# Performance work log

Hardware: AMD Instinct MI355X
Metric: run time of the kernel (lower is better)

Reference implementation:

```python
import jax, jax.numpy as jnp
import numpy as np

H = 8          # num_heads
DM = 128       # dmodel
BN_EPS = 1e-5


def _linear(x, w, b):
    # w stored as [in, out]
    return x @ w + b


def _relu_mha(q, k, v, qw, qb, kw, kb, vw, vb, ow, ob, mask):
    """TemMulHeadAtte: ReLU on projected Q/K/V, masked softmax, ReLU out-proj.
    q,k: [B,N,T,2*DM]; v: [B,N,T,DM]; mask: broadcastable to [B,N,H,T,T] or None."""
    B, N, T, _ = q.shape
    Q = jax.nn.relu(_linear(q, qw, qb)).reshape(B, N, T, H, -1)  # e = 2*DM/H
    K = jax.nn.relu(_linear(k, kw, kb)).reshape(B, N, T, H, -1)
    V = jax.nn.relu(_linear(v, vw, vb)).reshape(B, N, T, H, -1)  # d = DM/H
    scale = 1.0 / np.sqrt(Q.shape[-1]).astype(np.float32)
    scores = jnp.einsum('bnthe,bnshe->bnhts', Q, K)
    if mask is not None:
        scores = jnp.where(mask, -jnp.inf, scores)
    attn = jax.nn.softmax(scale * scores, axis=-1)  # dropout p=0 -> identity
    out = jnp.einsum('bnhts,bnshd->bnthd', attn, V).reshape(B, N, T, -1)
    return jax.nn.relu(_linear(out, ow, ob))


def setup_inputs() -> dict:
    key = jax.random.key(0)
    ks = iter(jax.random.split(key, 32))
    B, N, T = 16, 207, 24
    def w(shape, scale=0.05):
        return (jax.random.normal(next(ks), shape, dtype=jnp.float32) * scale)
    inp = {
        'x': w((B, N, T, DM), 1.0),
        'hidden': w((B, N, T, DM), 1.0),
        'tXin': w((B, N, T, DM), 1.0),
    }
    dk = 2 * DM // H * H   # 256
    dv = DM // H * H       # 128
    for pre in ('s', 't'):  # space / temporal attention params
        inp[pre + 'q_w'] = w((2 * DM, dk)); inp[pre + 'q_b'] = w((dk,))
        inp[pre + 'k_w'] = w((2 * DM, dk)); inp[pre + 'k_b'] = w((dk,))
        inp[pre + 'v_w'] = w((DM, dv));     inp[pre + 'v_b'] = w((dv,))
        inp[pre + 'o_w'] = w((dv, DM));     inp[pre + 'o_b'] = w((DM,))
    inp['gate_w'] = w((2 * DM, DM)); inp['gate_b'] = w((DM,))
    inp['bn_gamma'] = jnp.ones((DM,), jnp.float32)
    inp['bn_beta'] = jnp.zeros((DM,), jnp.float32)
    return inp


def reference(x, hidden, tXin,
              sq_w, sq_b, sk_w, sk_b, sv_w, sv_b, so_w, so_b,
              tq_w, tq_b, tk_w, tk_b, tv_w, tv_b, to_w, to_b,
              gate_w, gate_b, bn_gamma, bn_beta):
    B, N, T, E = hidden.shape
    ht = jnp.concatenate([hidden, tXin], axis=3)  # [B,N,T,2*DM]
    # spatial attention: attend over nodes (N<->T permute)
    sqk = ht.transpose(0, 2, 1, 3)        # [B,T,N,2*DM]
    sval = hidden.transpose(0, 2, 1, 3)   # [B,T,N,DM]
    spaceOut = _relu_mha(sqk, sqk, sval, sq_w, sq_b, sk_w, sk_b, sv_w, sv_b,
                         so_w, so_b, None).transpose(0, 2, 1, 3)  # [B,N,T,DM]
    # temporal attention with causal (strict upper-tri) mask
    mask = jnp.triu(jnp.ones((T, T), dtype=bool), 1)[None, None, None]
    tempOut = _relu_mha(ht, ht, hidden, tq_w, tq_b, tk_w, tk_b, tv_w, tv_b,
                        to_w, to_b, mask)  # [B,N,T,DM]
    # gate + BatchNorm2d over channel dim (training-mode batch stats, biased var)
    gi = _linear(jnp.concatenate([spaceOut, tempOut], axis=3), gate_w, gate_b)
    mean = gi.mean(axis=(0, 1, 2))
    var = gi.var(axis=(0, 1, 2))
    z = jax.nn.sigmoid((gi - mean) * jax.lax.rsqrt(var + BN_EPS) * bn_gamma + bn_beta)
    return z * spaceOut + (1.0 - z) * tempOut
```

## Files before the change

kernel.cpp:

```cpp
#include <hip/hip_runtime.h>
#include <hip/hip_bf16.h>

typedef __bf16 bf16;
typedef __bf16 bf16x8 __attribute__((ext_vector_type(8)));
typedef float f32x4 __attribute__((ext_vector_type(4)));

#define MTOT 79488
#define NDIM 207
#define TDIM 24

__global__ void detect_dtype(const void* __restrict__ hidden, int* __restrict__ flag)
{
    __shared__ int cnt;
    if (threadIdx.x == 0) cnt = 0;
    __syncthreads();
    const bf16* h = (const bf16*)hidden;
    int local = 0;
    for (int i = threadIdx.x; i < 4096; i += 256) {
        float v = (float)h[i];
        if (!(fabsf(v) < 1e6f)) local++;
    }
    atomicAdd(&cnt, local);
    __syncthreads();
    if (threadIdx.x == 0) *flag = (cnt > 8) ? 1 : 0;
}

__device__ inline float ld_ext(const void* p, int idx, int isF32)
{
    return isF32 ? ((const float*)p)[idx] : (float)((const bf16*)p)[idx];
}

__global__ __launch_bounds__(256) void cvt_inputs(
    const void* __restrict__ hidden, const void* __restrict__ tXin,
    bf16* __restrict__ hb, bf16* __restrict__ tb, const int* __restrict__ dtf)
{
    const int isF32 = *dtf;
    const void* src = blockIdx.y ? tXin : hidden;
    bf16* dst = blockIdx.y ? tb : hb;
    const size_t e8 = ((size_t)blockIdx.x * 256 + threadIdx.x) * 8;
    bf16x8 v;
    if (isF32) {
        f32x4 lo = *(const f32x4*)((const float*)src + e8);
        f32x4 hi = *(const f32x4*)((const float*)src + e8 + 4);
        v[0]=(bf16)lo[0]; v[1]=(bf16)lo[1]; v[2]=(bf16)lo[2]; v[3]=(bf16)lo[3];
        v[4]=(bf16)hi[0]; v[5]=(bf16)hi[1]; v[6]=(bf16)hi[2]; v[7]=(bf16)hi[3];
    } else {
        v = *(const bf16x8*)((const bf16*)src + e8);
    }
    *(bf16x8*)(dst + e8) = v;
}

__global__ __launch_bounds__(256) void prep_weights(
    const void* __restrict__ sq, const void* __restrict__ sk, const void* __restrict__ sv,
    const void* __restrict__ so, const void* __restrict__ tq, const void* __restrict__ tk,
    const void* __restrict__ tv, const void* __restrict__ to_, const void* __restrict__ gw,
    const void* __restrict__ sqb, const void* __restrict__ skb, const void* __restrict__ svb,
    const void* __restrict__ sob, const void* __restrict__ tqb, const void* __restrict__ tkb,
    const void* __restrict__ tvb, const void* __restrict__ tob, const void* __restrict__ gb,
    bf16* __restrict__ wdst, bf16* __restrict__ bdst, const int* __restrict__ dtf)
{
    const int isF32 = *dtf;
    if (blockIdx.x == 1536) {
        for (int j = threadIdx.x; j < 1664; j += 256) {
            const void* src; int i2;
            if      (j < 256)  { src = sqb; i2 = j; }
            else if (j < 512)  { src = skb; i2 = j - 256; }
            else if (j < 640)  { src = svb; i2 = j - 512; }
            else if (j < 896)  { src = tqb; i2 = j - 640; }
            else if (j < 1152) { src = tkb; i2 = j - 896; }
            else if (j < 1280) { src = tvb; i2 = j - 1152; }
            else if (j < 1408) { src = sob; i2 = j - 1280; }
            else if (j < 1536) { src = tob; i2 = j - 1408; }
            else               { src = gb;  i2 = j - 1536; }
            bdst[j] = (bf16)ld_ext(src, i2, isF32);
        }
        return;
    }
    const int e = blockIdx.x * 256 + threadIdx.x;
    float v;
    if (e < 327680) {
        int br = (e >= 163840);
        int e2 = e - br * 163840;
        int n = e2 >> 8, k = e2 & 255;
        const void* qw = br ? tq : sq;
        const void* kw = br ? tk : sk;
        const void* vw = br ? tv : sv;
        if      (n < 256) v = ld_ext(qw, k * 256 + n, isF32);
        else if (n < 512) v = ld_ext(kw, k * 256 + (n - 256), isF32);
        else              v = (k < 128) ? ld_ext(vw, k * 128 + (n - 512), isF32) : 0.f;
    } else if (e < 360448) {
        int br = (e >= 344064);
        int e2 = e - 327680 - br * 16384;
        int n = e2 >> 7, k = e2 & 127;
        v = ld_ext(br ? to_ : so, k * 128 + n, isF32);
    } else {
        int e2 = e - 360448;
        int n = e2 >> 8, k = e2 & 255;
        v = ld_ext(gw, k * 128 + n, isF32);
    }
    wdst[e] = (bf16)v;
}

__global__ __launch_bounds__(256) void gemm_bt(
    const void* __restrict__ A0v, const void* __restrict__ A1v,
    const bf16* __restrict__ Bt, const bf16* __restrict__ bias,
    bf16* __restrict__ C, int Nout, int Ktot, int doRelu, int aExt,
    const int* __restrict__ dtf)
{
    const int aF32 = aExt & *dtf;
    __shared__ bf16 As[128 * 72];
    __shared__ bf16 Bs[128 * 72];
    const int tid  = threadIdx.x;
    const int wid  = tid >> 6, lane = tid & 63;
    const int wm   = (wid >> 1) * 64, wn = (wid & 1) * 64;
    const int quad = lane >> 4, l16 = lane & 15;
    const int m0   = blockIdx.x * 128, n0 = blockIdx.y * 128;
    const int lrow = tid >> 3;
    const int lcol = (tid & 7) * 8;

    f32x4 acc[4][4] = {};

    for (int k0 = 0; k0 < Ktot; k0 += 64) {
        const void* Ap = (k0 < 128) ? A0v : A1v;
        const int koff = (k0 < 128) ? k0 : k0 - 128;
        #pragma unroll
        for (int p = 0; p < 4; ++p) {
            int r = lrow + p * 32;
            bf16x8 av;
            if (aF32) {
                const float* Af = (const float*)Ap;
                f32x4 lo = *(const f32x4*)(Af + (size_t)(m0 + r) * 128 + koff + lcol);
                f32x4 hi = *(const f32x4*)(Af + (size_t)(m0 + r) * 128 + koff + lcol + 4);
                av[0]=(bf16)lo[0]; av[1]=(bf16)lo[1]; av[2]=(bf16)lo[2]; av[3]=(bf16)lo[3];
                av[4]=(bf16)hi[0]; av[5]=(bf16)hi[1]; av[6]=(bf16)hi[2]; av[7]=(bf16)hi[3];
            } else {
                av = *(const bf16x8*)((const bf16*)Ap + (size_t)(m0 + r) * 128 + koff + lcol);
            }
            *(bf16x8*)&As[r * 72 + lcol] = av;
        }
        #pragma unroll
        for (int p = 0; p < 4; ++p) {
            int r = lrow + p * 32;
            *(bf16x8*)&Bs[r * 72 + lcol] =
                *(const bf16x8*)(Bt + (size_t)(n0 + r) * Ktot + k0 + lcol);
        }
        __syncthreads();
        #pragma unroll
        for (int kk = 0; kk < 64; kk += 32) {
            bf16x8 af[4], bfr[4];
            #pragma unroll
            for (int i = 0; i < 4; ++i)
                af[i] = *(const bf16x8*)&As[(wm + i * 16 + l16) * 72 + kk + quad * 8];
            #pragma unroll
            for (int j = 0; j < 4; ++j)
                bfr[j] = *(const bf16x8*)&Bs[(wn + j * 16 + l16) * 72 + kk + quad * 8];
            #pragma unroll
            for (int i = 0; i < 4; ++i)
                #pragma unroll
                for (int j = 0; j < 4; ++j)
                    acc[i][j] = __builtin_amdgcn_mfma_f32_16x16x32_bf16(
                        af[i], bfr[j], acc[i][j], 0, 0, 0);
        }
        __syncthreads();
    }
    #pragma unroll
    for (int j = 0; j < 4; ++j) {
        int col = n0 + wn + j * 16 + l16;
        float bv = (float)bias[col];
        #pragma unroll
        for (int i = 0; i < 4; ++i) {
            int rbase = m0 + wm + i * 16 + quad * 4;
            #pragma unroll
            for (int r = 0; r < 4; ++r) {
                float v = acc[i][j][r] + bv;
                if (doRelu) v = fmaxf(v, 0.f);
                C[(size_t)(rbase + r) * Nout + col] = (bf16)v;
            }
        }
    }
}

__global__ __launch_bounds__(256) void attn_spatial_mfma(
    const bf16* __restrict__ QKV, bf16* __restrict__ O)
{
    const int hh = blockIdx.x, t = blockIdx.y, b = blockIdx.z;
    __shared__ bf16 Ks[224 * 40];
    __shared__ bf16 Vt[16 * 232];
    __shared__ bf16 Pl[4][16 * 40];
    const int tid = threadIdx.x;
    const int wave = tid >> 6, lane = tid & 63;
    const int quad = lane >> 4, l16 = lane & 15;
    const int STR = 640;

    for (int idx = tid; idx < 224 * 4; idx += 256) {
        int n = idx >> 2, seg = (idx & 3) * 8;
        bf16x8 v8 = {};
        if (n < NDIM)
            v8 = *(const bf16x8*)(QKV + ((size_t)(b * NDIM + n) * TDIM + t) * STR
                                  + 256 + hh * 32 + seg);
        *(bf16x8*)&Ks[n * 40 + seg] = v8;
    }
    for (int idx = tid; idx < 224 * 16; idx += 256) {
        int s = idx >> 4, d = idx & 15;
        bf16 v = (bf16)0.f;
        if (s < NDIM)
            v = QKV[((size_t)(b * NDIM + s) * TDIM + t) * STR + 512 + hh * 16 + d];
        Vt[d * 232 + s] = v;
    }
    __syncthreads();

    const float scale = 0.17677669529663687f;

    for (int qt = wave; qt < 13; qt += 4) {
        const int q0 = qt * 16;
        int qrow = q0 + l16; if (qrow >= NDIM) qrow = NDIM - 1;
        bf16x8 qfrag = *(const bf16x8*)(QKV + ((size_t)(b * NDIM + qrow) * TDIM + t) * STR
                                        + hh * 32 + quad * 8);
        f32x4 s[14];
        #pragma unroll
        for (int c = 0; c < 14; ++c) {
            bf16x8 kf = *(const bf16x8*)&Ks[(c * 16 + l16) * 40 + quad * 8];
            f32x4 z = {};
            s[c] = __builtin_amdgcn_mfma_f32_16x16x32_bf16(qfrag, kf, z, 0, 0, 0);
        }
        float l[4];
        #pragma unroll
        for (int r = 0; r < 4; ++r) {
            float mx = -1e30f;
            #pragma unroll
            for (int c = 0; c < 14; ++c) {
                int si = c * 16 + l16;
                float x = (si < NDIM) ? s[c][r] : -1e30f;
                mx = fmaxf(mx, x);
            }
            mx = fmaxf(mx, __shfl_xor(mx, 1));
            mx = fmaxf(mx, __shfl_xor(mx, 2));
            mx = fmaxf(mx, __shfl_xor(mx, 4));
            mx = fmaxf(mx, __shfl_xor(mx, 8));
            float sum = 0.f;
            #pragma unroll
            for (int c = 0; c < 14; ++c) {
                int si = c * 16 + l16;
                float p = (si < NDIM) ? __expf((s[c][r] - mx) * scale) : 0.f;
                s[c][r] = p;
                sum += p;
            }
            sum += __shfl_xor(sum, 1);
            sum += __shfl_xor(sum, 2);
            sum += __shfl_xor(sum, 4);
            sum += __shfl_xor(sum, 8);
            l[r] = sum;
        }
        f32x4 oacc = {};
        #pragma unroll
        for (int sc = 0; sc < 7; ++sc) {
            #pragma unroll
            for (int r = 0; r < 4; ++r) {
                Pl[wave][(quad * 4 + r) * 40 + l16]      = (bf16)s[2 * sc][r];
                Pl[wave][(quad * 4 + r) * 40 + 16 + l16] = (bf16)s[2 * sc + 1][r];
            }
            bf16x8 pf = *(const bf16x8*)&Pl[wave][l16 * 40 + quad * 8];
            bf16x8 vf = *(const bf16x8*)&Vt[l16 * 232 + sc * 32 + quad * 8];
            oacc = __builtin_amdgcn_mfma_f32_16x16x32_bf16(pf, vf, oacc, 0, 0, 0);
        }
        #pragma unroll
        for (int r = 0; r < 4; ++r) {
            int row = q0 + quad * 4 + r;
            if (row < NDIM)
                O[((size_t)(b * NDIM + row) * TDIM + t) * 128 + hh * 16 + l16]
                    = (bf16)(oacc[r] / l[r]);
        }
    }
}

__global__ __launch_bounds__(256) void attn_temporal_mfma(
    const bf16* __restrict__ QKV, bf16* __restrict__ O)
{
    const size_t m0 = (size_t)blockIdx.x * TDIM;
    __shared__ bf16 Khs[8 * 32 * 40];
    __shared__ bf16 Vts[8 * 16 * 40];
    __shared__ bf16 Pl[4][16 * 40];
    const int tid = threadIdx.x;
    const int wave = tid >> 6, lane = tid & 63;
    const int quad = lane >> 4, l16 = lane & 15;
    const int STR = 640;

    for (int idx = tid; idx < 32 * 32; idx += 256) {
        int row = idx >> 5, seg = idx & 31;
        int h = seg >> 2, j = (seg & 3) * 8;
        bf16x8 v8 = {};
        if (row < TDIM)
            v8 = *(const bf16x8*)(QKV + (m0 + row) * STR + 256 + h * 32 + j);
        *(bf16x8*)&Khs[h * 1280 + row * 40 + j] = v8;
    }
    for (int idx = tid; idx < 32 * 128; idx += 256) {
        int s = idx >> 7, c = idx & 127;
        int h = c >> 4, d = c & 15;
        bf16 v = (bf16)0.f;
        if (s < TDIM) v = QKV[(m0 + s) * STR + 512 + h * 16 + d];
        Vts[h * 640 + d * 40 + s] = v;
    }
    __syncthreads();

    const float scale = 0.17677669529663687f;

    #pragma unroll
    for (int hi = 0; hi < 2; ++hi) {
        const int h = wave * 2 + hi;
        #pragma unroll
        for (int qt = 0; qt < 2; ++qt) {
            int qrow = qt * 16 + l16; if (qrow >= TDIM) qrow = TDIM - 1;
            bf16x8 qfrag = *(const bf16x8*)(QKV + (m0 + qrow) * STR + h * 32 + quad * 8);
            bf16x8 kf0 = *(const bf16x8*)&Khs[h * 1280 + l16 * 40 + quad * 8];
            bf16x8 kf1 = *(const bf16x8*)&Khs[h * 1280 + (16 + l16) * 40 + quad * 8];
            f32x4 z = {};
            f32x4 s0 = __builtin_amdgcn_mfma_f32_16x16x32_bf16(qfrag, kf0, z, 0, 0, 0);
            f32x4 s1 = __builtin_amdgcn_mfma_f32_16x16x32_bf16(qfrag, kf1, z, 0, 0, 0);
            float l[4];
            #pragma unroll
            for (int r = 0; r < 4; ++r) {
                int q = qt * 16 + quad * 4 + r;
                float x0 = (l16 <= q) ? s0[r] : -1e30f;
                float x1 = (16 + l16 <= q && 16 + l16 < TDIM) ? s1[r] : -1e30f;
                float mx = fmaxf(x0, x1);
                mx = fmaxf(mx, __shfl_xor(mx, 1));
                mx = fmaxf(mx, __shfl_xor(mx, 2));
                mx = fmaxf(mx, __shfl_xor(mx, 4));
                mx = fmaxf(mx, __shfl_xor(mx, 8));
                float p0 = (x0 > -1e29f) ? __expf((x0 - mx) * scale) : 0.f;
                float p1 = (x1 > -1e29f) ? __expf((x1 - mx) * scale) : 0.f;
                float sum = p0 + p1;
                sum += __shfl_xor(sum, 1);
                sum += __shfl_xor(sum, 2);
                sum += __shfl_xor(sum, 4);
                sum += __shfl_xor(sum, 8);
                l[r] = sum;
                Pl[wave][(quad * 4 + r) * 40 + l16]      = (bf16)p0;
                Pl[wave][(quad * 4 + r) * 40 + 16 + l16] = (bf16)p1;
            }
            bf16x8 pf = *(const bf16x8*)&Pl[wave][l16 * 40 + quad * 8];
            bf16x8 vf = *(const bf16x8*)&Vts[h * 640 + l16 * 40 + quad * 8];
            f32x4 oacc = __builtin_amdgcn_mfma_f32_16x16x32_bf16(pf, vf, z, 0, 0, 0);
            #pragma unroll
            for (int r = 0; r < 4; ++r) {
                int row = qt * 16 + quad * 4 + r;
                if (row < TDIM)
                    O[(m0 + row) * 128 + h * 16 + l16] = (bf16)(oacc[r] / l[r]);
            }
        }
    }
}

__global__ __launch_bounds__(256) void bn_stats(
    const bf16* __restrict__ gi, float* __restrict__ stats)
{
    __shared__ float ssum[256], ssq[256];
    const size_t base = (size_t)blockIdx.x * 16384;
    const int tid = threadIdx.x;
    float s = 0.f, sq = 0.f;
    #pragma unroll 4
    for (int i = 0; i < 64; ++i) {
        float v = (float)gi[base + (size_t)i * 256 + tid];
        s += v; sq += v * v;
    }
    ssum[tid] = s; ssq[tid] = sq;
    __syncthreads();
    if (tid < 128) {
        atomicAdd(&stats[tid], ssum[tid] + ssum[tid + 128]);
        atomicAdd(&stats[128 + tid], ssq[tid] + ssq[tid + 128]);
    }
}

__global__ __launch_bounds__(256) void bn_final(
    const bf16* __restrict__ gi, const bf16* __restrict__ sp, const bf16* __restrict__ tp,
    const void* __restrict__ gammav, const void* __restrict__ betav,
    const float* __restrict__ stats, void* __restrict__ outv,
    const int* __restrict__ dtf)
{
    const int isF32 = *dtf;
    const int idx = blockIdx.x * 256 + threadIdx.x;
    const int c = idx & 127;
    const float invM = 1.f / (float)MTOT;
    float mean = stats[c] * invM;
    float var  = stats[128 + c] * invM - mean * mean;
    float gam = ld_ext(gammav, c, isF32);
    float bet = ld_ext(betav, c, isF32);
    float g = (float)gi[idx];
    float zn = (g - mean) * rsqrtf(var + 1e-5f) * gam + bet;
    float z = 1.f / (1.f + __expf(-zn));
    float s = (float)sp[idx], t = (float)tp[idx];
    float r = z * s + (1.f - z) * t;
    if (isF32) ((float*)outv)[idx] = r;
    else       ((bf16*)outv)[idx] = (bf16)r;
}

extern "C" void kernel_launch(void* const* d_in, const int* in_sizes, int n_in,
                              void* d_out, int out_size, void* d_ws, size_t ws_size,
                              hipStream_t stream)
{
    const void* hidden = d_in[1];
    const void* tXin   = d_in[2];
    const void* sq_w = d_in[3];  const void* sq_b = d_in[4];
    const void* sk_w = d_in[5];  const void* sk_b = d_in[6];
    const void* sv_w = d_in[7];  const void* sv_b = d_in[8];
    const void* so_w = d_in[9];  const void* so_b = d_in[10];
    const void* tq_w = d_in[11]; const void* tq_b = d_in[12];
    const void* tk_w = d_in[13]; const void* tk_b = d_in[14];
    const void* tv_w = d_in[15]; const void* tv_b = d_in[16];
    const void* to_w = d_in[17]; const void* to_b = d_in[18];
    const void* gate_w = d_in[19]; const void* gate_b = d_in[20];
    const void* gamma  = d_in[21]; const void* beta   = d_in[22];

    char* ws = (char*)d_ws;
    float* stats = (float*)ws;
    int*  dtf    = (int*)(ws + 1024);
    bf16* bB     = (bf16*)(ws + 2048);
    bf16* wT     = (bf16*)(ws + 8192);
    bf16* spaceO = (bf16*)(ws + 794624);
    bf16* attnO  = (bf16*)(ws + 21143552);
    bf16* QKV    = (bf16*)(ws + 41492480);
    bf16* hb     = (bf16*)(ws + 143237120);
    bf16* tb     = (bf16*)(ws + 163586048);
    bf16* tempO  = attnO;
    bf16* gi     = QKV;

    const int wsBig = (ws_size >= 184000000ull);

    bf16* sW  = wT;            bf16* tW  = wT + 163840;
    bf16* soT = wT + 327680;   bf16* toT = wT + 344064;
    bf16* gwT = wT + 360448;

    hipMemsetAsync(stats, 0, 1024, stream);
    detect_dtype<<<1, 256, 0, stream>>>(hidden, dtf);
    prep_weights<<<dim3(1537), 256, 0, stream>>>(
        sq_w, sk_w, sv_w, so_w, tq_w, tk_w, tv_w, to_w, gate_w,
        sq_b, sk_b, sv_b, so_b, tq_b, tk_b, tv_b, to_b, gate_b,
        wT, bB, dtf);
    if (wsBig)
        cvt_inputs<<<dim3(4968, 2), 256, 0, stream>>>(hidden, tXin, hb, tb, dtf);

    const void* A0 = wsBig ? (const void*)hb : hidden;
    const void* A1 = wsBig ? (const void*)tb : tXin;
    const int aExt = wsBig ? 0 : 1;

    gemm_bt<<<dim3(621, 5), 256, 0, stream>>>(A0, A1, sW, bB, QKV, 640, 256, 1, aExt, dtf);
    attn_spatial_mfma<<<dim3(8, TDIM, 16), 256, 0, stream>>>(QKV, attnO);
    gemm_bt<<<dim3(621, 1), 256, 0, stream>>>(attnO, nullptr, soT, bB + 1280, spaceO, 128, 128, 1, 0, dtf);

    gemm_bt<<<dim3(621, 5), 256, 0, stream>>>(A0, A1, tW, bB + 640, QKV, 640, 256, 1, aExt, dtf);
    attn_temporal_mfma<<<dim3(16 * NDIM), 256, 0, stream>>>(QKV, attnO);
    gemm_bt<<<dim3(621, 1), 256, 0, stream>>>(attnO, nullptr, toT, bB + 1408, tempO, 128, 128, 1, 0, dtf);

    gemm_bt<<<dim3(621, 1), 256, 0, stream>>>(spaceO, tempO, gwT, bB + 1536, gi, 128, 256, 0, 0, dtf);
    bn_stats<<<dim3(621), 256, 0, stream>>>(gi, stats);
    bn_final<<<dim3(39744), 256, 0, stream>>>(gi, spaceO, tempO, gamma, beta, stats, d_out, dtf);
}
```

Before: 545.5 us.

## Permute GEMM outputs for spatial attention, fuse BN stats, drop softmax max

The spatial QKV GEMM now writes rows in [B,T,N] order so spatial attention reads contiguous node rows and loads V with vector loads, and the out-projection GEMM scatters back to [B,N,T]. BatchNorm sum and sum-of-squares are accumulated in the gate GEMM epilogue, which removes the separate bn_stats pass. Softmax skips the max subtraction and uses exp2 and reciprocal intrinsics, padding is trimmed, and bn_final is vectorised to 8 elements per thread. Dropping the max relies on ReLU-bounded scores staying small enough not to overflow exp, and permuted scattered stores may coalesce less well.

```diff
diff --git a/kernel.cpp b/kernel.cpp
--- a/kernel.cpp
+++ b/kernel.cpp
@@ -8,6 +8,8 @@
 #define MTOT 79488
 #define NDIM 207
 #define TDIM 24
+
+#define EXP2F(x) __builtin_amdgcn_exp2f(x)
 
 __global__ void detect_dtype(const void* __restrict__ hidden, int* __restrict__ flag)
 {
@@ -105,11 +107,12 @@
     const void* __restrict__ A0v, const void* __restrict__ A1v,
     const bf16* __restrict__ Bt, const bf16* __restrict__ bias,
     bf16* __restrict__ C, int Nout, int Ktot, int doRelu, int aExt,
-    const int* __restrict__ dtf)
+    const int* __restrict__ dtf, int permMode, float* __restrict__ stats)
 {
     const int aF32 = aExt & *dtf;
     __shared__ bf16 As[128 * 72];
     __shared__ bf16 Bs[128 * 72];
+    __shared__ float lsum[128], lsq[128];
     const int tid  = threadIdx.x;
     const int wid  = tid >> 6, lane = tid & 63;
     const int wm   = (wid >> 1) * 64, wn = (wid & 1) * 64;
@@ -163,19 +166,57 @@
         }
         __syncthreads();
     }
+
+    int orow[4][4];
+    #pragma unroll
+    for (int i = 0; i < 4; ++i)
+        #pragma unroll
+        for (int r = 0; r < 4; ++r) {
+            int m = m0 + wm + i * 16 + quad * 4 + r;
+            int o;
+            if (permMode == 1) {
+                int t = m % 24, bn = m / 24;
+                int n = bn % 207, b = bn / 207;
+                o = (b * 24 + t) * 207 + n;
+            } else if (permMode == 2) {
+                int n = m % 207, bt = m / 207;
+                int t = bt % 24, b = bt / 24;
+                o = (b * 207 + n) * 24 + t;
+            } else {
+                o = m;
+            }
+            orow[i][r] = o;
+        }
+
+    if (stats) {
+        if (tid < 128) { lsum[tid] = 0.f; lsq[tid] = 0.f; }
+        __syncthreads();
+    }
     #pragma unroll
     for (int j = 0; j < 4; ++j) {
         int col = n0 + wn + j * 16 + l16;
         float bv = (float)bias[col];
+        float ps = 0.f, psq = 0.f;
         #pragma unroll
         for (int i = 0; i < 4; ++i) {
-            int rbase = m0 + wm + i * 16 + quad * 4;
             #pragma unroll
             for (int r = 0; r < 4; ++r) {
                 float v = acc[i][j][r] + bv;
                 if (doRelu) v = fmaxf(v, 0.f);
-                C[(size_t)(rbase + r) * Nout + col] = (bf16)v;
-            }
+                if (stats) { ps += v; psq += v * v; }
+                C[(size_t)orow[i][r] * Nout + col] = (bf16)v;
+            }
+        }
+        if (stats) {
+            atomicAdd(&lsum[col & 127], ps);
+            atomicAdd(&lsq[col & 127], psq);
+        }
+    }
+    if (stats) {
+        __syncthreads();
+        if (tid < 128) {
+            atomicAdd(&stats[tid], lsum[tid]);
+            atomicAdd(&stats[128 + tid], lsq[tid]);
         }
     }
 }
@@ -184,64 +225,53 @@
     const bf16* __restrict__ QKV, bf16* __restrict__ O)
 {
     const int hh = blockIdx.x, t = blockIdx.y, b = blockIdx.z;
-    __shared__ bf16 Ks[224 * 40];
+    __shared__ bf16 Ks[208 * 40];
     __shared__ bf16 Vt[16 * 232];
-    __shared__ bf16 Pl[4][16 * 40];
+    __shared__ bf16 Pl[4][2][16 * 40];
     const int tid = threadIdx.x;
     const int wave = tid >> 6, lane = tid & 63;
     const int quad = lane >> 4, l16 = lane & 15;
-    const int STR = 640;
-
-    for (int idx = tid; idx < 224 * 4; idx += 256) {
+    const size_t R = (size_t)(b * TDIM + t) * NDIM;
+
+    for (int idx = tid; idx < 832; idx += 256) {
         int n = idx >> 2, seg = (idx & 3) * 8;
         bf16x8 v8 = {};
         if (n < NDIM)
-            v8 = *(const bf16x8*)(QKV + ((size_t)(b * NDIM + n) * TDIM + t) * STR
-                                  + 256 + hh * 32 + seg);
+            v8 = *(const bf16x8*)(QKV + (R + n) * 640 + 256 + hh * 32 + seg);
         *(bf16x8*)&Ks[n * 40 + seg] = v8;
     }
-    for (int idx = tid; idx < 224 * 16; idx += 256) {
-        int s = idx >> 4, d = idx & 15;
-        bf16 v = (bf16)0.f;
+    for (int idx = tid; idx < 448; idx += 256) {
+        int s = idx >> 1, half = (idx & 1) * 8;
+        bf16x8 v8 = {};
         if (s < NDIM)
-            v = QKV[((size_t)(b * NDIM + s) * TDIM + t) * STR + 512 + hh * 16 + d];
-        Vt[d * 232 + s] = v;
+            v8 = *(const bf16x8*)(QKV + (R + s) * 640 + 512 + hh * 16 + half);
+        #pragma unroll
+        for (int j = 0; j < 8; ++j)
+            Vt[(half + j) * 232 + s] = v8[j];
     }
     __syncthreads();
 
-    const float scale = 0.17677669529663687f;
+    const float k2 = 0.25506538410868237f;
 
     for (int qt = wave; qt < 13; qt += 4) {
         const int q0 = qt * 16;
         int qrow = q0 + l16; if (qrow >= NDIM) qrow = NDIM - 1;
-        bf16x8 qfrag = *(const bf16x8*)(QKV + ((size_t)(b * NDIM + qrow) * TDIM + t) * STR
-                                        + hh * 32 + quad * 8);
-        f32x4 s[14];
-        #pragma unroll
-        for (int c = 0; c < 14; ++c) {
+        bf16x8 qfrag = *(const bf16x8*)(QKV + (R + qrow) * 640 + hh * 32 + quad * 8);
+        f32x4 s[13];
+        #pragma unroll
+        for (int c = 0; c < 13; ++c) {
             bf16x8 kf = *(const bf16x8*)&Ks[(c * 16 + l16) * 40 + quad * 8];
             f32x4 z = {};
             s[c] = __builtin_amdgcn_mfma_f32_16x16x32_bf16(qfrag, kf, z, 0, 0, 0);
         }
-        float l[4];
+        float linv[4];
         #pragma unroll
         for (int r = 0; r < 4; ++r) {
-            float mx = -1e30f;
-            #pragma unroll
-            for (int c = 0; c < 14; ++c) {
-                int si = c * 16 + l16;
-                float x = (si < NDIM) ? s[c][r] : -1e30f;
-                mx = fmaxf(mx, x);
-            }
-            mx = fmaxf(mx, __shfl_xor(mx, 1));
-            mx = fmaxf(mx, __shfl_xor(mx, 2));
-            mx = fmaxf(mx, __shfl_xor(mx, 4));
-            mx = fmaxf(mx, __shfl_xor(mx, 8));
             float sum = 0.f;
             #pragma unroll
-            for (int c = 0; c < 14; ++c) {
-                int si = c * 16 + l16;
-                float p = (si < NDIM) ? __expf((s[c][r] - mx) * scale) : 0.f;
+            for (int c = 0; c < 13; ++c) {
+                float p = EXP2F(s[c][r] * k2);
+                if (c == 12 && l16 == 15) p = 0.f;
                 s[c][r] = p;
                 sum += p;
             }
@@ -249,17 +279,20 @@
             sum += __shfl_xor(sum, 2);
             sum += __shfl_xor(sum, 4);
             sum += __shfl_xor(sum, 8);
-            l[r] = sum;
+            linv[r] = __builtin_amdgcn_rcpf(sum);
         }
         f32x4 oacc = {};
         #pragma unroll
         for (int sc = 0; sc < 7; ++sc) {
+            bf16* pb = &Pl[wave][sc & 1][0];
             #pragma unroll
             for (int r = 0; r < 4; ++r) {
-                Pl[wave][(quad * 4 + r) * 40 + l16]      = (bf16)s[2 * sc][r];
-                Pl[wave][(quad * 4 + r) * 40 + 16 + l16] = (bf16)s[2 * sc + 1][r];
-            }
-            bf16x8 pf = *(const bf16x8*)&Pl[wave][l16 * 40 + quad * 8];
+                float p1 = 0.f;
+                if (sc < 6) p1 = s[2 * sc + 1][r];
+                pb[(quad * 4 + r) * 40 + l16]      = (bf16)s[2 * sc][r];
+                pb[(quad * 4 + r) * 40 + 16 + l16] = (bf16)p1;
+            }
+            bf16x8 pf = *(const bf16x8*)&pb[l16 * 40 + quad * 8];
             bf16x8 vf = *(const bf16x8*)&Vt[l16 * 232 + sc * 32 + quad * 8];
             oacc = __builtin_amdgcn_mfma_f32_16x16x32_bf16(pf, vf, oacc, 0, 0, 0);
         }
@@ -267,8 +300,7 @@
         for (int r = 0; r < 4; ++r) {
             int row = q0 + quad * 4 + r;
             if (row < NDIM)
-                O[((size_t)(b * NDIM + row) * TDIM + t) * 128 + hh * 16 + l16]
-                    = (bf16)(oacc[r] / l[r]);
+                O[(R + row) * 128 + hh * 16 + l16] = (bf16)(oacc[r] * linv[r]);
         }
     }
 }
@@ -279,7 +311,7 @@
     const size_t m0 = (size_t)blockIdx.x * TDIM;
     __shared__ bf16 Khs[8 * 32 * 40];
     __shared__ bf16 Vts[8 * 16 * 40];
-    __shared__ bf16 Pl[4][16 * 40];
+    __shared__ bf16 Pl[4][2][16 * 40];
     const int tid = threadIdx.x;
     const int wave = tid >> 6, lane = tid & 63;
     const int quad = lane >> 4, l16 = lane & 15;
@@ -302,7 +334,7 @@
     }
     __syncthreads();
 
-    const float scale = 0.17677669529663687f;
+    const float k2 = 0.25506538410868237f;
 
     #pragma unroll
     for (int hi = 0; hi < 2; ++hi) {
@@ -316,58 +348,32 @@
             f32x4 z = {};
             f32x4 s0 = __builtin_amdgcn_mfma_f32_16x16x32_bf16(qfrag, kf0, z, 0, 0, 0);
             f32x4 s1 = __builtin_amdgcn_mfma_f32_16x16x32_bf16(qfrag, kf1, z, 0, 0, 0);
-            float l[4];
+            bf16* pb = &Pl[wave][qt][0];
+            float linv[4];
             #pragma unroll
             for (int r = 0; r < 4; ++r) {
                 int q = qt * 16 + quad * 4 + r;
-                float x0 = (l16 <= q) ? s0[r] : -1e30f;
-                float x1 = (16 + l16 <= q && 16 + l16 < TDIM) ? s1[r] : -1e30f;
-                float mx = fmaxf(x0, x1);
-                mx = fmaxf(mx, __shfl_xor(mx, 1));
-                mx = fmaxf(mx, __shfl_xor(mx, 2));
-                mx = fmaxf(mx, __shfl_xor(mx, 4));
-                mx = fmaxf(mx, __shfl_xor(mx, 8));
-                float p0 = (x0 > -1e29f) ? __expf((x0 - mx) * scale) : 0.f;
-                float p1 = (x1 > -1e29f) ? __expf((x1 - mx) * scale) : 0.f;
+                float p0 = (l16 <= q)      ? EXP2F(s0[r] * k2) : 0.f;
+                float p1 = (16 + l16 <= q) ? EXP2F(s1[r] * k2) : 0.f;
                 float sum = p0 + p1;
                 sum += __shfl_xor(sum, 1);
                 sum += __shfl_xor(sum, 2);
                 sum += __shfl_xor(sum, 4);
                 sum += __shfl_xor(sum, 8);
-                l[r] = sum;
-                Pl[wave][(quad * 4 + r) * 40 + l16]      = (bf16)p0;
-                Pl[wave][(quad * 4 + r) * 40 + 16 + l16] = (bf16)p1;
-            }
-            bf16x8 pf = *(const bf16x8*)&Pl[wave][l16 * 40 + quad * 8];
+                linv[r] = __builtin_amdgcn_rcpf(sum);
+                pb[(quad * 4 + r) * 40 + l16]      = (bf16)p0;
+                pb[(quad * 4 + r) * 40 + 16 + l16] = (bf16)p1;
+            }
+            bf16x8 pf = *(const bf16x8*)&pb[l16 * 40 + quad * 8];
             bf16x8 vf = *(const bf16x8*)&Vts[h * 640 + l16 * 40 + quad * 8];
             f32x4 oacc = __builtin_amdgcn_mfma_f32_16x16x32_bf16(pf, vf, z, 0, 0, 0);
             #pragma unroll
             for (int r = 0; r < 4; ++r) {
                 int row = qt * 16 + quad * 4 + r;
                 if (row < TDIM)
-                    O[(m0 + row) * 128 + h * 16 + l16] = (bf16)(oacc[r] / l[r]);
-            }
-        }
-    }
-}
-
-__global__ __launch_bounds__(256) void bn_stats(
-    const bf16* __restrict__ gi, float* __restrict__ stats)
-{
-    __shared__ float ssum[256], ssq[256];
-    const size_t base = (size_t)blockIdx.x * 16384;
-    const int tid = threadIdx.x;
-    float s = 0.f, sq = 0.f;
-    #pragma unroll 4
-    for (int i = 0; i < 64; ++i) {
-        float v = (float)gi[base + (size_t)i * 256 + tid];
-        s += v; sq += v * v;
-    }
-    ssum[tid] = s; ssq[tid] = sq;
-    __syncthreads();
-    if (tid < 128) {
-        atomicAdd(&stats[tid], ssum[tid] + ssum[tid + 128]);
-        atomicAdd(&stats[128 + tid], ssq[tid] + ssq[tid + 128]);
+                    O[(m0 + row) * 128 + h * 16 + l16] = (bf16)(oacc[r] * linv[r]);
+            }
+        }
     }
 }
 
@@ -378,20 +384,38 @@
     const int* __restrict__ dtf)
 {
     const int isF32 = *dtf;
-    const int idx = blockIdx.x * 256 + threadIdx.x;
-    const int c = idx & 127;
+    const size_t base = ((size_t)blockIdx.x * 256 + threadIdx.x) * 8;
+    const int c0 = (int)(base & 127);
     const float invM = 1.f / (float)MTOT;
-    float mean = stats[c] * invM;
-    float var  = stats[128 + c] * invM - mean * mean;
-    float gam = ld_ext(gammav, c, isF32);
-    float bet = ld_ext(betav, c, isF32);
-    float g = (float)gi[idx];
-    float zn = (g - mean) * rsqrtf(var + 1e-5f) * gam + bet;
-    float z = 1.f / (1.f + __expf(-zn));
-    float s = (float)sp[idx], t = (float)tp[idx];
-    float r = z * s + (1.f - z) * t;
-    if (isF32) ((float*)outv)[idx] = r;
-    else       ((bf16*)outv)[idx] = (bf16)r;
+    bf16x8 g8 = *(const bf16x8*)(gi + base);
+    bf16x8 s8 = *(const bf16x8*)(sp + base);
+    bf16x8 t8 = *(const bf16x8*)(tp + base);
+    float res[8];
+    #pragma unroll
+    for (int j = 0; j < 8; ++j) {
+        int c = c0 + j;
+        float mean = stats[c] * invM;
+        float var  = stats[128 + c] * invM - mean * mean;
+        float gam = ld_ext(gammav, c, isF32);
+        float bet = ld_ext(betav, c, isF32);
+        float g = (float)g8[j];
+        float zn = (g - mean) * rsqrtf(var + 1e-5f) * gam + bet;
+        float z = 1.f / (1.f + EXP2F(zn * -1.4426950408889634f));
+        float sv = (float)s8[j], tv = (float)t8[j];
+        res[j] = z * sv + (1.f - z) * tv;
+    }
+    if (isF32) {
+        float* op = (float*)outv + base;
+        f32x4 lo = {res[0], res[1], res[2], res[3]};
+        f32x4 hi = {res[4], res[5], res[6], res[7]};
+        *(f32x4*)op = lo;
+        *(f32x4*)(op + 4) = hi;
+    } else {
+        bf16x8 o8;
+        #pragma unroll
+        for (int j = 0; j < 8; ++j) o8[j] = (bf16)res[j];
+        *(bf16x8*)((bf16*)outv + base) = o8;
+    }
 }
 
 extern "C" void kernel_launch(void* const* d_in, const int* in_sizes, int n_in,
@@ -430,7 +454,7 @@
     bf16* soT = wT + 327680;   bf16* toT = wT + 344064;
     bf16* gwT = wT + 360448;
 
-    hipMemsetAsync(stats, 0, 1024, stream);
+    (void)hipMemsetAsync(stats, 0, 1024, stream);
     detect_dtype<<<1, 256, 0, stream>>>(hidden, dtf);
     prep_weights<<<dim3(1537), 256, 0, stream>>>(
         sq_w, sk_w, sv_w, so_w, tq_w, tk_w, tv_w, to_w, gate_w,
@@ -443,15 +467,14 @@
     const void* A1 = wsBig ? (const void*)tb : tXin;
     const int aExt = wsBig ? 0 : 1;
 
-    gemm_bt<<<dim3(621, 5), 256, 0, stream>>>(A0, A1, sW, bB, QKV, 640, 256, 1, aExt, dtf);
+    gemm_bt<<<dim3(621, 5), 256, 0, stream>>>(A0, A1, sW, bB, QKV, 640, 256, 1, aExt, dtf, 1, nullptr);
     attn_spatial_mfma<<<dim3(8, TDIM, 16), 256, 0, stream>>>(QKV, attnO);
-    gemm_bt<<<dim3(621, 1), 256, 0, stream>>>(attnO, nullptr, soT, bB + 1280, spaceO, 128, 128, 1, 0, dtf);
-
-    gemm_bt<<<dim3(621, 5), 256, 0, stream>>>(A0, A1, tW, bB + 640, QKV, 640, 256, 1, aExt, dtf);
+    gemm_bt<<<dim3(621, 1), 256, 0, stream>>>(attnO, nullptr, soT, bB + 1280, spaceO, 128, 128, 1, 0, dtf, 2, nullptr);
+
+    gemm_bt<<<dim3(621, 5), 256, 0, stream>>>(A0, A1, tW, bB + 640, QKV, 640, 256, 1, aExt, dtf, 0, nullptr);
     attn_temporal_mfma<<<dim3(16 * NDIM), 256, 0, stream>>>(QKV, attnO);
-    gemm_bt<<<dim3(621, 1), 256, 0, stream>>>(attnO, nullptr, toT, bB + 1408, tempO, 128, 128, 1, 0, dtf);
-
-    gemm_bt<<<dim3(621, 1), 256, 0, stream>>>(spaceO, tempO, gwT, bB + 1536, gi, 128, 256, 0, 0, dtf);
-    bn_stats<<<dim3(621), 256, 0, stream>>>(gi, stats);
-    bn_final<<<dim3(39744), 256, 0, stream>>>(gi, spaceO, tempO, gamma, beta, stats, d_out, dtf);
-}
+    gemm_bt<<<dim3(621, 1), 256, 0, stream>>>(attnO, nullptr, toT, bB + 1408, tempO, 128, 128, 1, 0, dtf, 0, nullptr);
+
+    gemm_bt<<<dim3(621, 1), 256, 0, stream>>>(spaceO, tempO, gwT, bB + 1536, gi, 128, 256, 0, 0, dtf, 0, stats);
+    bn_final<<<dim3(4968), 256, 0, stream>>>(gi, spaceO, tempO, gamma, beta, stats, d_out, dtf);
+}
```

Result: slower. 563.9 us (+3.4%).
